# Optimization experiments

Measured on AMD Instinct MI355X. Metric: run time of the kernel, lower is better.

Reference implementation:

```python
import jax, jax.numpy as jnp
import numpy as np

# Module constants from __init__: z_max=32, ppm=2 -> delta=0.5, z_min=delta=0.5, log_prob=True
Z_MIN = 0.5
Z_MAX = 32.0
DELTA = 0.5


def _depth_positions(S):
    # depth_steps = arange(z_min, z_max + delta, delta) -> Z=64 bins in [0.5, 32]
    depth_steps = jnp.arange(Z_MIN, Z_MAX + DELTA, DELTA)
    log_steps = jnp.log2(depth_steps)
    log_min = np.log2(Z_MIN)
    log_max = np.log2(Z_MAX)
    norm = (log_steps - log_min) / (log_max - log_min)  # in [0, 1]
    # grid_sample align_corners=True maps [-1,1] -> [0, S-1]; norm*2-1 -> norm*(S-1)
    return norm * (S - 1)  # (Z,)


def setup_inputs() -> dict:
    key = jax.random.key(0)
    k1, k2 = jax.random.split(key)
    image = jax.random.normal(k1, (32, 64, 64, 128), dtype=jnp.float32)          # (B,D,H,W)
    polar_log_depths = jax.random.normal(k2, (32, 64, 128, 64), dtype=jnp.float32)  # (B,H,W,S)
    return {"image": image, "polar_log_depths": polar_log_depths}


def reference(image, polar_log_depths):
    S = polar_log_depths.shape[-1]
    pos = _depth_positions(S)                                 # (Z,) fixed interp positions
    i0 = jnp.clip(jnp.floor(pos).astype(jnp.int32), 0, S - 1)
    i1 = jnp.clip(i0 + 1, 0, S - 1)
    w = pos - i0.astype(pos.dtype)                            # linear weights; w=0 at right edge
    v0 = jnp.take(polar_log_depths, i0, axis=-1)              # (B,H,W,Z)
    v1 = jnp.take(polar_log_depths, i1, axis=-1)
    depth_scores = v0 * (1.0 - w) + v1 * w                    # 1D linear interp == grid_sample here

    # log_prob=True branch: softmax / logsumexp over height axis (dim=1)
    depth_prob = jax.nn.softmax(depth_scores, axis=1)         # (B,H,W,Z)
    cell_score = jax.nn.logsumexp(depth_scores, axis=1)       # (B,W,Z)

    # einsum '...dhw,...hwz->...dzw': weighted reduction over height
    image_polar = jnp.einsum('bdhw,bhwz->bdzw', image, depth_prob)  # (B,D,Z,W)
    return image_polar, cell_score
```

## Files before the change

kernel.cpp:

```cpp
#include <hip/hip_runtime.h>
#include <hip/hip_bf16.h>
#include <math.h>

#define B_ 32
#define D_ 64
#define H_ 64
#define W_ 128
#define S_ 64
#define Z_ 64
#define WT 4

typedef __attribute__((ext_vector_type(8))) short bf16x8;
typedef __attribute__((ext_vector_type(4))) float f32x4;

static __device__ __forceinline__ short f2bf(float f) {
    union { __hip_bfloat16 h; short s; } u;
    u.h = __float2bfloat16(f);
    return u.s;
}

__global__ __launch_bounds__(256, 2)
void polar_proj_kernel(const float* __restrict__ image,
                       const float* __restrict__ polar,
                       float* __restrict__ out_img,
                       float* __restrict__ out_cell) {
    __shared__ __align__(16) unsigned char sP[WT * 64 * 128];
    __shared__ __align__(16) unsigned char sA[WT * 64 * 128];

    const int t = threadIdx.x;

    const int cpx = gridDim.x >> 3;
    const int logical = (blockIdx.x & 7) * cpx + (blockIdx.x >> 3);
    const int b  = logical >> 5;
    const int w0 = (logical & 31) << 2;

    const int h_im = t & 63;
    const int dq   = t >> 6;
    float4 ireg[16];
#pragma unroll
    for (int j = 0; j < 16; ++j) {
        const int d = dq + 4 * j;
        ireg[j] = *(const float4*)(image + ((size_t)((b * D_ + d) * H_ + h_im)) * W_ + w0);
    }

    const int q  = t & 3;
    const int r2 = t >> 2;
    float4 preg[16];
#pragma unroll
    for (int p = 0; p < 4; ++p) {
        const int rr = p * 64 + r2;
        const int w  = rr >> 6, h = rr & 63;
        const float* src = polar + ((size_t)((b * H_ + h) * W_ + w0 + w)) * S_ + q * 16;
#pragma unroll
        for (int k = 0; k < 4; ++k)
            preg[p * 4 + k] = *(const float4*)(src + k * 4);
    }
#pragma unroll
    for (int p = 0; p < 4; ++p) {
        const int rr = p * 64 + r2;
        const int w  = rr >> 6, h = rr & 63;
#pragma unroll
        for (int c = 0; c < 2; ++c) {
            bf16x8 v;
#pragma unroll
            for (int e = 0; e < 8; ++e)
                v[e] = f2bf(((const float*)&preg[p * 4 + c * 2 + (e >> 2)])[e & 3]);
            *(bf16x8*)(sP + w * 8192 + h * 128 + ((((q << 1) | c) ^ (h & 7)) << 4)) = v;
        }
    }
    __syncthreads();

    const int wi = t & 3;
    const int z  = t >> 2;
    const float posf = (log2f(0.5f + 0.5f * (float)z) + 1.0f) * 10.5f;
    int i0 = (int)floorf(posf);
    i0 = i0 < 0 ? 0 : (i0 > S_ - 1 ? S_ - 1 : i0);
    const int i1 = (i0 + 1 > S_ - 1) ? (S_ - 1) : (i0 + 1);
    const float wq = posf - (float)i0;

    const unsigned char* base0 = sP + wi * 8192 + ((i0 & 7) << 1);
    const unsigned char* base1 = sP + wi * 8192 + ((i1 & 7) << 1);
    const int sx0 = (i0 >> 3) << 4;
    const int sx1 = (i1 >> 3) << 4;
    const unsigned char* p0[8];
    const unsigned char* p1[8];
#pragma unroll
    for (int hc = 0; hc < 8; ++hc) {
        p0[hc] = base0 + (sx0 ^ (hc << 4));
        p1[hc] = base1 + (sx1 ^ (hc << 4));
    }

    float sc[64];
    float mx[4] = {-1e30f, -1e30f, -1e30f, -1e30f};
#pragma unroll
    for (int h = 0; h < 64; ++h) {
        const float v0 = __bfloat162float(*(const __hip_bfloat16*)(p0[h & 7] + h * 128));
        const float v1 = __bfloat162float(*(const __hip_bfloat16*)(p1[h & 7] + h * 128));
        const float v = v0 + wq * (v1 - v0);
        sc[h] = v;
        mx[h & 3] = fmaxf(mx[h & 3], v);
    }
    const float m = fmaxf(fmaxf(mx[0], mx[1]), fmaxf(mx[2], mx[3]));
    float sm[4] = {0.f, 0.f, 0.f, 0.f};
#pragma unroll
    for (int h = 0; h < 64; ++h) {
        const float e = __expf(sc[h] - m);
        sc[h] = e;
        sm[h & 3] += e;
    }
    const float s = (sm[0] + sm[1]) + (sm[2] + sm[3]);
    out_cell[((size_t)b * W_ + w0 + wi) * Z_ + z] = m + logf(s);
    const float inv = 1.0f / s;
    __syncthreads();

#pragma unroll
    for (int j = 0; j < 8; ++j) {
        bf16x8 v;
#pragma unroll
        for (int e = 0; e < 8; ++e)
            v[e] = f2bf(sc[j * 8 + e] * inv);
        *(bf16x8*)(sP + wi * 8192 + z * 128 + ((j ^ (z & 7)) << 4)) = v;
    }
#pragma unroll
    for (int j = 0; j < 16; ++j) {
        const int d = dq + 4 * j;
        unsigned char* dst = sA + d * 128 + (((h_im >> 3) ^ (d & 7)) << 4) + ((h_im & 7) << 1);
#pragma unroll
        for (int w = 0; w < 4; ++w)
            *(short*)(dst + w * 8192) = f2bf(((const float*)&ireg[j])[w]);
    }
    __syncthreads();

    const int lane = t & 63;
    const int wv   = t >> 6;
    const int fr   = lane & 15;
    const int lg   = lane >> 4;
    const int rowA = wv * 16 + fr;
    const int fx   = (fr & 7) << 4;

    f32x4 acc[4][4] = {};
#pragma unroll
    for (int w = 0; w < 4; ++w) {
        const unsigned char* aw = sA + w * 8192 + rowA * 128;
        const bf16x8 a0 = *(const bf16x8*)(aw + ((lg << 4) ^ fx));
        const bf16x8 a1 = *(const bf16x8*)(aw + (((4 + lg) << 4) ^ fx));
#pragma unroll
        for (int nt = 0; nt < 4; ++nt) {
            const unsigned char* bw = sP + w * 8192 + (nt * 16 + fr) * 128;
            const bf16x8 b0 = *(const bf16x8*)(bw + ((lg << 4) ^ fx));
            const bf16x8 b1 = *(const bf16x8*)(bw + (((4 + lg) << 4) ^ fx));
            acc[w][nt] = __builtin_amdgcn_mfma_f32_16x16x32_bf16(a0, b0, acc[w][nt], 0, 0, 0);
            acc[w][nt] = __builtin_amdgcn_mfma_f32_16x16x32_bf16(a1, b1, acc[w][nt], 0, 0, 0);
        }
    }

#pragma unroll
    for (int nt = 0; nt < 4; ++nt)
#pragma unroll
        for (int r = 0; r < 4; ++r) {
            float4 o;
            o.x = acc[0][nt][r];
            o.y = acc[1][nt][r];
            o.z = acc[2][nt][r];
            o.w = acc[3][nt][r];
            const int d = wv * 16 + lg * 4 + r;
            const int zc = nt * 16 + fr;
            *(float4*)(out_img + ((size_t)((b * D_ + d) * Z_) + zc) * W_ + w0) = o;
        }
}

extern "C" void kernel_launch(void* const* d_in, const int* in_sizes, int n_in,
                              void* d_out, int out_size, void* d_ws, size_t ws_size,
                              hipStream_t stream) {
    const float* image = (const float*)d_in[0];
    const float* polar = (const float*)d_in[1];
    float* out_img  = (float*)d_out;
    float* out_cell = out_img + (size_t)B_ * D_ * Z_ * W_;
    dim3 grid(B_ * (W_ / WT));
    polar_proj_kernel<<<grid, 256, 0, stream>>>(image, polar, out_img, out_cell);
}
```

Before: 56.01 us.

## Widen W tile to 8 with 1024-thread blocks and LDS-staged coalesced output

New measurement: 53.91 us. -3.7%, faster.

```diff
diff --git a/kernel.cpp b/kernel.cpp
--- a/kernel.cpp
+++ b/kernel.cpp
@@ -8,7 +8,7 @@
 #define W_ 128
 #define S_ 64
 #define Z_ 64
-#define WT 4
+#define WT 8
 
 typedef __attribute__((ext_vector_type(8))) short bf16x8;
 typedef __attribute__((ext_vector_type(4))) float f32x4;
@@ -19,154 +19,172 @@
     return u.s;
 }
 
-__global__ __launch_bounds__(256, 2)
+static __device__ __forceinline__ int swz(int w, int row, int oct) {
+    return w * 8192 + row * 128 + (((oct ^ row ^ w) & 7) << 4);
+}
+
+__global__ __launch_bounds__(1024, 4)
 void polar_proj_kernel(const float* __restrict__ image,
                        const float* __restrict__ polar,
                        float* __restrict__ out_img,
                        float* __restrict__ out_cell) {
-    __shared__ __align__(16) unsigned char sP[WT * 64 * 128];
-    __shared__ __align__(16) unsigned char sA[WT * 64 * 128];
+    __shared__ __align__(16) unsigned char sP[WT * 8192];
+    __shared__ __align__(16) unsigned char sA[WT * 8192];
 
     const int t = threadIdx.x;
 
     const int cpx = gridDim.x >> 3;
     const int logical = (blockIdx.x & 7) * cpx + (blockIdx.x >> 3);
-    const int b  = logical >> 5;
-    const int w0 = (logical & 31) << 2;
+    const int b  = logical >> 4;
+    const int w0 = (logical & 15) << 3;
 
-    const int h_im = t & 63;
-    const int dq   = t >> 6;
-    float4 ireg[16];
+    const int wq = t & 1;
+    float4 ir[8];
 #pragma unroll
-    for (int j = 0; j < 16; ++j) {
-        const int d = dq + 4 * j;
-        ireg[j] = *(const float4*)(image + ((size_t)((b * D_ + d) * H_ + h_im)) * W_ + w0);
+    for (int i = 0; i < 8; ++i) {
+        const int p = i * 512 + (t >> 1);
+        const int d = p >> 6, h = p & 63;
+        ir[i] = *(const float4*)(image + ((size_t)((b * D_ + d) * H_ + h)) * W_ + w0 + wq * 4);
     }
 
-    const int q  = t & 3;
-    const int r2 = t >> 2;
-    float4 preg[16];
+    const int q4 = t & 3;
+    const int rbase = t >> 2;
+    float4 pr[8];
 #pragma unroll
-    for (int p = 0; p < 4; ++p) {
-        const int rr = p * 64 + r2;
-        const int w  = rr >> 6, h = rr & 63;
-        const float* src = polar + ((size_t)((b * H_ + h) * W_ + w0 + w)) * S_ + q * 16;
+    for (int rp = 0; rp < 2; ++rp) {
+        const int rr = rbase + rp * 256;
+        const int w = rr >> 6, h = rr & 63;
+        const float* src = polar + ((size_t)((b * H_ + h) * W_ + w0 + w)) * S_ + q4 * 16;
 #pragma unroll
         for (int k = 0; k < 4; ++k)
-            preg[p * 4 + k] = *(const float4*)(src + k * 4);
+            pr[rp * 4 + k] = *(const float4*)(src + k * 4);
     }
+
 #pragma unroll
-    for (int p = 0; p < 4; ++p) {
-        const int rr = p * 64 + r2;
-        const int w  = rr >> 6, h = rr & 63;
+    for (int i = 0; i < 8; ++i) {
+        const int p = i * 512 + (t >> 1);
+        const int d = p >> 6, h = p & 63;
+#pragma unroll
+        for (int c = 0; c < 4; ++c) {
+            const int w = wq * 4 + c;
+            *(short*)(sA + swz(w, d, h >> 3) + ((h & 7) << 1)) = f2bf(((const float*)&ir[i])[c]);
+        }
+    }
+
+#pragma unroll
+    for (int rp = 0; rp < 2; ++rp) {
+        const int rr = rbase + rp * 256;
+        const int w = rr >> 6, h = rr & 63;
 #pragma unroll
         for (int c = 0; c < 2; ++c) {
             bf16x8 v;
 #pragma unroll
             for (int e = 0; e < 8; ++e)
-                v[e] = f2bf(((const float*)&preg[p * 4 + c * 2 + (e >> 2)])[e & 3]);
-            *(bf16x8*)(sP + w * 8192 + h * 128 + ((((q << 1) | c) ^ (h & 7)) << 4)) = v;
+                v[e] = f2bf(((const float*)&pr[rp * 4 + c * 2 + (e >> 2)])[e & 3]);
+            *(bf16x8*)(sP + swz(w, h, q4 * 2 + c)) = v;
         }
     }
     __syncthreads();
 
-    const int wi = t & 3;
-    const int z  = t >> 2;
-    const float posf = (log2f(0.5f + 0.5f * (float)z) + 1.0f) * 10.5f;
+    const int wsm  = t >> 7;
+    const int zsm  = (t >> 1) & 63;
+    const int half = t & 1;
+    const float posf = (log2f(0.5f + 0.5f * (float)zsm) + 1.0f) * 10.5f;
     int i0 = (int)floorf(posf);
     i0 = i0 < 0 ? 0 : (i0 > S_ - 1 ? S_ - 1 : i0);
     const int i1 = (i0 + 1 > S_ - 1) ? (S_ - 1) : (i0 + 1);
-    const float wq = posf - (float)i0;
+    const float wqf = posf - (float)i0;
 
-    const unsigned char* base0 = sP + wi * 8192 + ((i0 & 7) << 1);
-    const unsigned char* base1 = sP + wi * 8192 + ((i1 & 7) << 1);
-    const int sx0 = (i0 >> 3) << 4;
-    const int sx1 = (i1 >> 3) << 4;
+    const unsigned char* pl = sP + wsm * 8192;
+    const int lo0 = (i0 & 7) << 1, lo1 = (i1 & 7) << 1;
     const unsigned char* p0[8];
     const unsigned char* p1[8];
 #pragma unroll
     for (int hc = 0; hc < 8; ++hc) {
-        p0[hc] = base0 + (sx0 ^ (hc << 4));
-        p1[hc] = base1 + (sx1 ^ (hc << 4));
+        p0[hc] = pl + ((((i0 >> 3) ^ hc ^ wsm) & 7) << 4) + lo0;
+        p1[hc] = pl + ((((i1 >> 3) ^ hc ^ wsm) & 7) << 4) + lo1;
     }
 
-    float sc[64];
-    float mx[4] = {-1e30f, -1e30f, -1e30f, -1e30f};
+    float e[32];
+    float mx0 = -1e30f, mx1 = -1e30f;
 #pragma unroll
-    for (int h = 0; h < 64; ++h) {
-        const float v0 = __bfloat162float(*(const __hip_bfloat16*)(p0[h & 7] + h * 128));
-        const float v1 = __bfloat162float(*(const __hip_bfloat16*)(p1[h & 7] + h * 128));
-        const float v = v0 + wq * (v1 - v0);
-        sc[h] = v;
-        mx[h & 3] = fmaxf(mx[h & 3], v);
+    for (int j = 0; j < 32; ++j) {
+        const int h = half * 32 + j;
+        const float v0 = __bfloat162float(*(const __hip_bfloat16*)(p0[j & 7] + h * 128));
+        const float v1 = __bfloat162float(*(const __hip_bfloat16*)(p1[j & 7] + h * 128));
+        const float v = v0 + wqf * (v1 - v0);
+        e[j] = v;
+        if (j & 1) mx1 = fmaxf(mx1, v); else mx0 = fmaxf(mx0, v);
     }
-    const float m = fmaxf(fmaxf(mx[0], mx[1]), fmaxf(mx[2], mx[3]));
-    float sm[4] = {0.f, 0.f, 0.f, 0.f};
+    float m = fmaxf(mx0, mx1);
+    m = fmaxf(m, __shfl_xor(m, 1));
+    float s0 = 0.f, s1 = 0.f;
 #pragma unroll
-    for (int h = 0; h < 64; ++h) {
-        const float e = __expf(sc[h] - m);
-        sc[h] = e;
-        sm[h & 3] += e;
+    for (int j = 0; j < 32; ++j) {
+        const float ev = __expf(e[j] - m);
+        e[j] = ev;
+        if (j & 1) s1 += ev; else s0 += ev;
     }
-    const float s = (sm[0] + sm[1]) + (sm[2] + sm[3]);
-    out_cell[((size_t)b * W_ + w0 + wi) * Z_ + z] = m + logf(s);
+    float s = s0 + s1;
+    s += __shfl_xor(s, 1);
+    if (half == 0)
+        out_cell[((size_t)b * W_ + w0 + wsm) * Z_ + zsm] = m + logf(s);
     const float inv = 1.0f / s;
     __syncthreads();
 
 #pragma unroll
-    for (int j = 0; j < 8; ++j) {
+    for (int c = 0; c < 4; ++c) {
         bf16x8 v;
 #pragma unroll
-        for (int e = 0; e < 8; ++e)
-            v[e] = f2bf(sc[j * 8 + e] * inv);
-        *(bf16x8*)(sP + wi * 8192 + z * 128 + ((j ^ (z & 7)) << 4)) = v;
-    }
-#pragma unroll
-    for (int j = 0; j < 16; ++j) {
-        const int d = dq + 4 * j;
-        unsigned char* dst = sA + d * 128 + (((h_im >> 3) ^ (d & 7)) << 4) + ((h_im & 7) << 1);
-#pragma unroll
-        for (int w = 0; w < 4; ++w)
-            *(short*)(dst + w * 8192) = f2bf(((const float*)&ireg[j])[w]);
+        for (int ee = 0; ee < 8; ++ee)
+            v[ee] = f2bf(e[c * 8 + ee] * inv);
+        *(bf16x8*)(sP + swz(wsm, zsm, half * 4 + c)) = v;
     }
     __syncthreads();
 
     const int lane = t & 63;
     const int wv   = t >> 6;
-    const int fr   = lane & 15;
-    const int lg   = lane >> 4;
-    const int rowA = wv * 16 + fr;
-    const int fx   = (fr & 7) << 4;
+    const int mt   = wv >> 2, nt = wv & 3;
+    const int fr   = lane & 15, lg = lane >> 4;
+    const int rowA = mt * 16 + fr;
+    const int rowB = nt * 16 + fr;
 
-    f32x4 acc[4][4] = {};
+    f32x4 acc[8] = {};
 #pragma unroll
-    for (int w = 0; w < 4; ++w) {
-        const unsigned char* aw = sA + w * 8192 + rowA * 128;
-        const bf16x8 a0 = *(const bf16x8*)(aw + ((lg << 4) ^ fx));
-        const bf16x8 a1 = *(const bf16x8*)(aw + (((4 + lg) << 4) ^ fx));
+    for (int w = 0; w < 8; ++w)
 #pragma unroll
-        for (int nt = 0; nt < 4; ++nt) {
-            const unsigned char* bw = sP + w * 8192 + (nt * 16 + fr) * 128;
-            const bf16x8 b0 = *(const bf16x8*)(bw + ((lg << 4) ^ fx));
-            const bf16x8 b1 = *(const bf16x8*)(bw + (((4 + lg) << 4) ^ fx));
-            acc[w][nt] = __builtin_amdgcn_mfma_f32_16x16x32_bf16(a0, b0, acc[w][nt], 0, 0, 0);
-            acc[w][nt] = __builtin_amdgcn_mfma_f32_16x16x32_bf16(a1, b1, acc[w][nt], 0, 0, 0);
+        for (int ks = 0; ks < 2; ++ks) {
+            const bf16x8 a  = *(const bf16x8*)(sA + swz(w, rowA, ks * 4 + lg));
+            const bf16x8 bb = *(const bf16x8*)(sP + swz(w, rowB, ks * 4 + lg));
+            acc[w] = __builtin_amdgcn_mfma_f32_16x16x32_bf16(a, bb, acc[w], 0, 0, 0);
+        }
+    __syncthreads();
+
+    unsigned char* rg = (wv & 8) ? (sA + (wv & 7) * 8192) : (sP + (wv & 7) * 8192);
+#pragma unroll
+    for (int r = 0; r < 4; ++r) {
+        const int li = fr * 4 + lg + r * 64;
+#pragma unroll
+        for (int wp = 0; wp < 4; ++wp) {
+            float2 v;
+            v.x = acc[wp * 2][r];
+            v.y = acc[wp * 2 + 1][r];
+            *(float2*)(rg + li * 32 + wp * 8) = v;
         }
     }
-
+    __syncthreads();
+    const unsigned char* rgc = rg;
 #pragma unroll
-    for (int nt = 0; nt < 4; ++nt)
-#pragma unroll
-        for (int r = 0; r < 4; ++r) {
-            float4 o;
-            o.x = acc[0][nt][r];
-            o.y = acc[1][nt][r];
-            o.z = acc[2][nt][r];
-            o.w = acc[3][nt][r];
-            const int d = wv * 16 + lg * 4 + r;
-            const int zc = nt * 16 + fr;
-            *(float4*)(out_img + ((size_t)((b * D_ + d) * Z_) + zc) * W_ + w0) = o;
-        }
+    for (int i = 0; i < 8; ++i) {
+        const int dz = (lane >> 1) + i * 32;
+        const int wh = lane & 1;
+        const int di = dz >> 4, zi = dz & 15;
+        const int li = zi * 4 + (di >> 2) + (di & 3) * 64;
+        const float4 v = *(const float4*)(rgc + li * 32 + wh * 16);
+        const int d = mt * 16 + di;
+        const int z = nt * 16 + zi;
+        *(float4*)(out_img + ((size_t)((b * D_ + d) * Z_) + z) * W_ + w0 + wh * 4) = v;
+    }
 }
 
 extern "C" void kernel_launch(void* const* d_in, const int* in_sizes, int n_in,
@@ -177,5 +195,5 @@
     float* out_img  = (float*)d_out;
     float* out_cell = out_img + (size_t)B_ * D_ * Z_ * W_;
     dim3 grid(B_ * (W_ / WT));
-    polar_proj_kernel<<<grid, 256, 0, stream>>>(image, polar, out_img, out_cell);
+    polar_proj_kernel<<<grid, 1024, 0, stream>>>(image, polar, out_img, out_cell);
 }
```
